# Performance work log

Hardware: AMD Instinct MI355X
Metric: run time of the kernel (lower is better)

## Reference

```python
import jax, jax.numpy as jnp
import numpy as np

B, N, D, H = 4, 2048, 768, 12
HD = D // H  # head_dim = 64


def setup_inputs() -> dict:
    key = jax.random.key(0)
    k1, k2, k3 = jax.random.split(key, 3)
    z = jax.random.normal(k1, (B, N, D), dtype=jnp.float32)
    # per-head qkv Linear weights, torch Linear convention: y = x @ W.T + b
    Wqkv = jax.random.normal(k2, (H, 3 * HD, D), dtype=jnp.float32) * 0.02
    bqkv = jnp.zeros((H, 3 * HD), dtype=jnp.float32)
    Wmsa = jax.random.normal(k3, (D, D), dtype=jnp.float32) * 0.02
    bmsa = jnp.zeros((D,), dtype=jnp.float32)
    return {"z": z, "Wqkv": Wqkv, "bqkv": bqkv, "Wmsa": Wmsa, "bmsa": bmsa}


def reference(z, Wqkv, bqkv, Wmsa, bmsa):
    # All heads' qkv projections in one einsum: [B,N,D] x [H,3hd,D] -> [B,H,N,3hd]
    qkv = jnp.einsum("bnd,hed->bhne", z, Wqkv) + bqkv[None, :, None, :]
    q, k, v = jnp.split(qkv, 3, axis=-1)  # each [B,H,N,hd]
    scale = 1.0 / jnp.sqrt(jnp.asarray(HD, dtype=z.dtype))
    scores = jnp.einsum("bhqd,bhkd->bhqk", q, k) * scale  # [B,H,N,N]
    attn = jax.nn.softmax(scores, axis=-1)
    out = jnp.einsum("bhqk,bhkd->bhqd", attn, v)  # [B,H,N,hd]
    # concat heads (head order matches the torch per-head cat)
    out = out.transpose(0, 2, 1, 3).reshape(B, N, H * HD)  # [B,N,D]
    return out @ Wmsa.T + bmsa
```

## Files before the change

kernel.cpp:

```cpp
#include <hip/hip_runtime.h>

typedef unsigned short u16;
typedef unsigned int u32;
typedef __attribute__((ext_vector_type(8))) short bf16x8;
typedef __attribute__((ext_vector_type(4))) float f32x4;

#define B_ 4
#define H_ 12
#define N_ 2048
#define D_ 768
#define HD_ 64
#define NTOK (B_ * N_)
#define NE   (H_ * 3 * HD_)

#define BM 128
#define BN 128
#define BK 64

#define QSCALE 0.18033688011112042f

__device__ __forceinline__ u16 f2bf(float f) {
    u32 u = __float_as_uint(f);
    u += 0x7fffu + ((u >> 16) & 1u);
    return (u16)(u >> 16);
}

__device__ __forceinline__ f32x4 mfma16(bf16x8 a, bf16x8 b, f32x4 c) {
    return __builtin_amdgcn_mfma_f32_16x16x32_bf16(a, b, c, 0, 0, 0);
}

__device__ __forceinline__ void g2l16(const u16* g, u16* l) {
    __builtin_amdgcn_global_load_lds(
        (const __attribute__((address_space(1))) void*)g,
        (__attribute__((address_space(3))) void*)l, 16, 0, 0);
}

__global__ __launch_bounds__(256) void cvt_bf16(const float* __restrict__ in,
                                                u16* __restrict__ out, int n4) {
    int i = blockIdx.x * blockDim.x + threadIdx.x;
    if (i < n4) {
        float4 v = ((const float4*)in)[i];
        u32 lo = (u32)f2bf(v.x) | ((u32)f2bf(v.y) << 16);
        u32 hi = (u32)f2bf(v.z) | ((u32)f2bf(v.w) << 16);
        ((uint2*)out)[i] = make_uint2(lo, hi);
    }
}

#define GEMM_CORE(Xp, Wp)                                                      \
    __shared__ u16 ldsA[BM * BK];                                              \
    __shared__ u16 ldsB[BN * BK];                                              \
    const int tid = threadIdx.x;                                               \
    const int wave = tid >> 6, lane = tid & 63;                                \
    const int lrow = lane & 15, quad = lane >> 4;                              \
    const int mbase = blockIdx.x * BM;                                         \
    const int nbase = blockIdx.y * BN;                                         \
    const int srow = tid >> 3;                                      \
    const int schunk = tid & 7;                                                \
    const int sk = (schunk ^ (srow & 7)) << 3;   \
    const int sdst = srow * BK + schunk * 8;     \
    const u16* gA = Xp + (size_t)(mbase + srow) * D_ + sk;                     \
    const u16* gB = Wp + (size_t)(nbase + srow) * D_ + sk;                     \
    const int m_ofs = (wave >> 1) * 64;                                        \
    const int n_ofs = (wave & 1) * 64;                                         \
    const int e_ = lrow & 7;                                                   \
    const int offA0 = (m_ofs + lrow) * BK + ((quad ^ e_) << 3);                \
    const int offB0 = (n_ofs + lrow) * BK + ((quad ^ e_) << 3);                \
    f32x4 acc[4][4] = {};                                                      \
    for (int kt = 0; kt < D_; kt += BK) {                                      \
        __syncthreads();                                                       \
        _Pragma("unroll") for (int i = 0; i < 4; i++) {                        \
            g2l16(gA + (size_t)(32 * i) * D_ + kt, ldsA + sdst + i * 32 * BK); \
            g2l16(gB + (size_t)(32 * i) * D_ + kt, ldsB + sdst + i * 32 * BK); \
        }                                                                      \
        __syncthreads();                                                       \
        _Pragma("unroll") for (int ks = 0; ks < 2; ks++) {                     \
            const int oa = offA0 ^ (ks << 5);                                  \
            const int ob = offB0 ^ (ks << 5);                                  \
            bf16x8 af[4], bfr[4];                                              \
            _Pragma("unroll") for (int c = 0; c < 4; c++)                      \
                af[c] = *(const bf16x8*)&ldsA[oa + c * 16 * BK];               \
            _Pragma("unroll") for (int c = 0; c < 4; c++)                      \
                bfr[c] = *(const bf16x8*)&ldsB[ob + c * 16 * BK];              \
            _Pragma("unroll") for (int i = 0; i < 4; i++)                      \
                _Pragma("unroll") for (int j = 0; j < 4; j++)                  \
                    acc[i][j] = mfma16(af[i], bfr[j], acc[i][j]);              \
        }                                                                      \
    }

__global__ __launch_bounds__(256) void gemm_qkv(const u16* __restrict__ X,
                                                const u16* __restrict__ W,
                                                const float* __restrict__ bqkv,
                                                u16* __restrict__ Qs,
                                                u16* __restrict__ Ks,
                                                u16* __restrict__ Vt) {
    GEMM_CORE(X, W)
#pragma unroll
    for (int cn = 0; cn < 4; cn++) {
        const int E = nbase + n_ofs + cn * 16;
        const int h = E / 192;
        const int rr = E - h * 192;
        const int kind = rr >> 6;
        const int d = (rr & 63) + lrow;
        const float bias = bqkv[E + lrow];
#pragma unroll
        for (int cm = 0; cm < 4; cm++) {
#pragma unroll
            for (int r = 0; r < 4; r++) {
                const int t = mbase + m_ofs + cm * 16 + quad * 4 + r;
                const int b_ = t >> 11, n = t & (N_ - 1);
                const size_t bh = (size_t)(b_ * H_ + h);
                const float val = acc[cm][cn][r] + bias;
                if (kind == 0) {
                    Qs[(bh * N_ + n) * HD_ + d] = f2bf(val * QSCALE);
                } else if (kind == 1) {
                    Ks[(bh * N_ + n) * HD_ + d] = f2bf(val);
                } else {
                    Vt[(bh * HD_ + d) * N_ + n] = f2bf(val);
                }
            }
        }
    }
}

__global__ __launch_bounds__(256) void gemm_out(const u16* __restrict__ X2,
                                                const u16* __restrict__ W,
                                                const float* __restrict__ bmsa,
                                                float* __restrict__ out) {
    GEMM_CORE(X2, W)
#pragma unroll
    for (int cn = 0; cn < 4; cn++) {
        const int col = nbase + n_ofs + cn * 16 + lrow;
        const float bias = bmsa[col];
#pragma unroll
        for (int cm = 0; cm < 4; cm++) {
#pragma unroll
            for (int r = 0; r < 4; r++) {
                const int t = mbase + m_ofs + cm * 16 + quad * 4 + r;
                out[(size_t)t * D_ + col] = acc[cm][cn][r] + bias;
            }
        }
    }
}

__global__ __launch_bounds__(256, 3) void flash_attn(const u16* __restrict__ Qs,
                                                     const u16* __restrict__ Ks,
                                                     const u16* __restrict__ Vt,
                                                     u16* __restrict__ X2) {
    __shared__ u16 ldsK[2][64 * HD_];
    __shared__ u16 ldsV[2][64 * HD_];
    __shared__ u16 ldsP[4][2][16][68];
    const int tid = threadIdx.x;
    const int wave = tid >> 6, lane = tid & 63;
    const int lrow = lane & 15, quad = lane >> 4;
    const int qbase = blockIdx.x * 128 + wave * 32;
    const int bh = blockIdx.y;
    const int b = bh / H_, h = bh - b * H_;

    const u16* Kb = Ks + (size_t)bh * N_ * HD_;
    const u16* Vb = Vt + (size_t)bh * HD_ * N_;

    const int srow = tid >> 3;
    const int schunk = tid & 7;
    const int skk = (schunk ^ (srow & 7)) << 3;
    const int sdst = srow * HD_ + schunk * 8;

    bf16x8 qa[2][2];
#pragma unroll
    for (int t = 0; t < 2; t++) {
        const u16* Qb = Qs + ((size_t)bh * N_ + qbase + t * 16 + lrow) * HD_ + quad * 8;
        qa[t][0] = *(const bf16x8*)(Qb);
        qa[t][1] = *(const bf16x8*)(Qb + 32);
    }

    const int fofs = (quad ^ (lrow & 7)) << 3;
    const short onebf = (short)0x3F80;
    const bf16x8 ones = {onebf, onebf, onebf, onebf, onebf, onebf, onebf, onebf};

    f32x4 Oacc[2][4] = {};
    f32x4 lacc[2] = {};

    {
        const u16* gK = Kb + (size_t)srow * HD_ + skk;
        g2l16(gK, &ldsK[0][sdst]);
        g2l16(gK + (size_t)32 * HD_, &ldsK[0][sdst + 32 * HD_]);
        const u16* gV = Vb + (size_t)srow * N_ + skk;
        g2l16(gV, &ldsV[0][sdst]);
        g2l16(gV + (size_t)32 * N_, &ldsV[0][sdst + 32 * HD_]);
    }

    for (int it = 0; it < N_ / 64; it++) {
        const int cur = it & 1;
        __syncthreads();
        if (it + 1 < N_ / 64) {
            const int kt2 = (it + 1) << 6;
            const u16* gK = Kb + (size_t)(kt2 + srow) * HD_ + skk;
            g2l16(gK, &ldsK[cur ^ 1][sdst]);
            g2l16(gK + (size_t)32 * HD_, &ldsK[cur ^ 1][sdst + 32 * HD_]);
            const u16* gV = Vb + (size_t)srow * N_ + kt2 + skk;
            g2l16(gV, &ldsV[cur ^ 1][sdst]);
            g2l16(gV + (size_t)32 * N_, &ldsV[cur ^ 1][sdst + 32 * HD_]);
        }
        bf16x8 kf[8];
#pragma unroll
        for (int c = 0; c < 4; c++) {
            const int o = (c * 16 + lrow) * HD_ + fofs;
            kf[2 * c]     = *(const bf16x8*)&ldsK[cur][o];
            kf[2 * c + 1] = *(const bf16x8*)&ldsK[cur][o ^ 32];
        }
        f32x4 s[2][4] = {};
#pragma unroll
        for (int t = 0; t < 2; t++)
#pragma unroll
            for (int c = 0; c < 4; c++) {
                s[t][c] = mfma16(kf[2 * c], qa[t][0], s[t][c]);
                s[t][c] = mfma16(kf[2 * c + 1], qa[t][1], s[t][c]);
            }
#pragma unroll
        for (int t = 0; t < 2; t++)
#pragma unroll
            for (int c = 0; c < 4; c++) {
                u32 a0 = __float_as_uint(__builtin_amdgcn_exp2f(s[t][c][0])) + 0x8000u;
                u32 a1 = __float_as_uint(__builtin_amdgcn_exp2f(s[t][c][1])) + 0x8000u;
                u32 a2 = __float_as_uint(__builtin_amdgcn_exp2f(s[t][c][2])) + 0x8000u;
                u32 a3 = __float_as_uint(__builtin_amdgcn_exp2f(s[t][c][3])) + 0x8000u;
                uint2 pk;
                pk.x = __builtin_amdgcn_perm(a1, a0, 0x07060302u);
                pk.y = __builtin_amdgcn_perm(a3, a2, 0x07060302u);
                *(uint2*)&ldsP[wave][t][lrow][c * 16 + quad * 4] = pk;
            }
        bf16x8 pa[2][2];
#pragma unroll
        for (int t = 0; t < 2; t++) {
            pa[t][0] = *(const bf16x8*)&ldsP[wave][t][lrow][quad * 8];
            pa[t][1] = *(const bf16x8*)&ldsP[wave][t][lrow][32 + quad * 8];
        }
#pragma unroll
        for (int t = 0; t < 2; t++) {
            lacc[t] = mfma16(pa[t][0], ones, lacc[t]);
            lacc[t] = mfma16(pa[t][1], ones, lacc[t]);
        }
#pragma unroll
        for (int c = 0; c < 4; c++) {
            const int o = (c * 16 + lrow) * HD_ + fofs;
            bf16x8 v0 = *(const bf16x8*)&ldsV[cur][o];
            bf16x8 v1 = *(const bf16x8*)&ldsV[cur][o ^ 32];
#pragma unroll
            for (int t = 0; t < 2; t++) {
                Oacc[t][c] = mfma16(pa[t][0], v0, Oacc[t][c]);
                Oacc[t][c] = mfma16(pa[t][1], v1, Oacc[t][c]);
            }
        }
    }
#pragma unroll
    for (int t = 0; t < 2; t++)
#pragma unroll
        for (int r = 0; r < 4; r++) {
            const float inv = 1.0f / lacc[t][r];
            const int qrow = qbase + t * 16 + quad * 4 + r;
#pragma unroll
            for (int c = 0; c < 4; c++) {
                X2[((size_t)b * N_ + qrow) * D_ + h * HD_ + c * 16 + lrow] =
                    f2bf(Oacc[t][c][r] * inv);
            }
        }
}

extern "C" void kernel_launch(void* const* d_in, const int* in_sizes, int n_in,
                              void* d_out, int out_size, void* d_ws, size_t ws_size,
                              hipStream_t stream) {
    const float* z    = (const float*)d_in[0];
    const float* Wqkv = (const float*)d_in[1];
    const float* bqkv = (const float*)d_in[2];
    const float* Wmsa = (const float*)d_in[3];
    const float* bmsa = (const float*)d_in[4];
    float* out = (float*)d_out;

    u16* Xbf = (u16*)d_ws;
    u16* Wqb = Xbf + (size_t)NTOK * D_;
    u16* Wmb = Wqb + (size_t)NE * D_;
    u16* Qs  = Wmb + (size_t)D_ * D_;
    u16* Ks  = Qs + (size_t)B_ * H_ * N_ * HD_;
    u16* Vt  = Ks + (size_t)B_ * H_ * N_ * HD_;
    u16* X2  = Vt + (size_t)B_ * H_ * N_ * HD_;

    const int nz = NTOK * D_ / 4;
    const int nwq = NE * D_ / 4;
    const int nwm = D_ * D_ / 4;
    cvt_bf16<<<(nz + 255) / 256, 256, 0, stream>>>(z, Xbf, nz);
    cvt_bf16<<<(nwq + 255) / 256, 256, 0, stream>>>(Wqkv, Wqb, nwq);
    cvt_bf16<<<(nwm + 255) / 256, 256, 0, stream>>>(Wmsa, Wmb, nwm);

    gemm_qkv<<<dim3(NTOK / BM, NE / BN), 256, 0, stream>>>(Xbf, Wqb, bqkv, Qs, Ks, Vt);
    flash_attn<<<dim3(N_ / 128, B_ * H_), 256, 0, stream>>>(Qs, Ks, Vt, X2);
    gemm_out<<<dim3(NTOK / BM, D_ / BN), 256, 0, stream>>>(X2, Wmb, bmsa, out);
}
```

Before: 228.9 us.

## Fuse bf16 conversions, stage QKV epilogue through LDS, shrink out-GEMM tile

The three fp32→bf16 conversion launches become one kernel that indexes across all three buffers. The QKV GEMM epilogue now stages the Q and K tiles in padded LDS and writes them as full 128-byte row vectors instead of scattered 2-byte stores. V^T is written as packed 8-byte chunks. The output GEMM uses 64-row tiles, doubling its block count for better occupancy across CUs at the cost of less reuse of the B operand.

Result: faster. 215.3 us (-6.0%).

```diff
diff --git a/kernel.cpp b/kernel.cpp
--- a/kernel.cpp
+++ b/kernel.cpp
@@ -13,9 +13,8 @@
 #define NTOK (B_ * N_)
 #define NE   (H_ * 3 * HD_)
 
-#define BM 128
-#define BN 128
 #define BK 64
+#define CPITCH 144
 
 #define QSCALE 0.18033688011112042f
 
@@ -35,53 +34,71 @@
         (__attribute__((address_space(3))) void*)l, 16, 0, 0);
 }
 
-__global__ __launch_bounds__(256) void cvt_bf16(const float* __restrict__ in,
-                                                u16* __restrict__ out, int n4) {
+#define NZ4  (NTOK * D_ / 4)
+#define NWQ4 (NE * D_ / 4)
+#define NWM4 (D_ * D_ / 4)
+__global__ __launch_bounds__(256) void cvt_all(const float* __restrict__ z,
+                                               const float* __restrict__ Wq,
+                                               const float* __restrict__ Wm,
+                                               u16* __restrict__ Xbf,
+                                               u16* __restrict__ Wqb,
+                                               u16* __restrict__ Wmb) {
     int i = blockIdx.x * blockDim.x + threadIdx.x;
-    if (i < n4) {
-        float4 v = ((const float4*)in)[i];
-        u32 lo = (u32)f2bf(v.x) | ((u32)f2bf(v.y) << 16);
-        u32 hi = (u32)f2bf(v.z) | ((u32)f2bf(v.w) << 16);
-        ((uint2*)out)[i] = make_uint2(lo, hi);
-    }
-}
-
-#define GEMM_CORE(Xp, Wp)                                                      \
-    __shared__ u16 ldsA[BM * BK];                                              \
-    __shared__ u16 ldsB[BN * BK];                                              \
+    const float* src;
+    u16* dst;
+    int j;
+    if (i < NZ4) {
+        src = z; dst = Xbf; j = i;
+    } else if (i < NZ4 + NWQ4) {
+        src = Wq; dst = Wqb; j = i - NZ4;
+    } else if (i < NZ4 + NWQ4 + NWM4) {
+        src = Wm; dst = Wmb; j = i - NZ4 - NWQ4;
+    } else {
+        return;
+    }
+    float4 v = ((const float4*)src)[j];
+    u32 lo = (u32)f2bf(v.x) | ((u32)f2bf(v.y) << 16);
+    u32 hi = (u32)f2bf(v.z) | ((u32)f2bf(v.w) << 16);
+    ((uint2*)dst)[j] = make_uint2(lo, hi);
+}
+
+#define GEMM_CORE(Xp, Wp, TM, SMELEMS)                                         \
+    __shared__ u16 smem[SMELEMS];                                              \
+    u16* ldsA = smem;                                                          \
+    u16* ldsB = smem + (TM) * BK;                                              \
     const int tid = threadIdx.x;                                               \
     const int wave = tid >> 6, lane = tid & 63;                                \
     const int lrow = lane & 15, quad = lane >> 4;                              \
-    const int mbase = blockIdx.x * BM;                                         \
-    const int nbase = blockIdx.y * BN;                                         \
+    const int mbase = blockIdx.x * (TM);                                       \
+    const int nbase = blockIdx.y * 128;                                        \
     const int srow = tid >> 3;                                      \
     const int schunk = tid & 7;                                                \
     const int sk = (schunk ^ (srow & 7)) << 3;   \
     const int sdst = srow * BK + schunk * 8;     \
     const u16* gA = Xp + (size_t)(mbase + srow) * D_ + sk;                     \
     const u16* gB = Wp + (size_t)(nbase + srow) * D_ + sk;                     \
-    const int m_ofs = (wave >> 1) * 64;                                        \
+    const int m_ofs = (wave >> 1) * ((TM) / 2);                                \
     const int n_ofs = (wave & 1) * 64;                                         \
     const int e_ = lrow & 7;                                                   \
     const int offA0 = (m_ofs + lrow) * BK + ((quad ^ e_) << 3);                \
     const int offB0 = (n_ofs + lrow) * BK + ((quad ^ e_) << 3);                \
-    f32x4 acc[4][4] = {};                                                      \
+    f32x4 acc[(TM) / 32][4] = {};                                              \
     for (int kt = 0; kt < D_; kt += BK) {                                      \
         __syncthreads();                                                       \
-        _Pragma("unroll") for (int i = 0; i < 4; i++) {                        \
+        _Pragma("unroll") for (int i = 0; i < (TM) / 32; i++)                  \
             g2l16(gA + (size_t)(32 * i) * D_ + kt, ldsA + sdst + i * 32 * BK); \
+        _Pragma("unroll") for (int i = 0; i < 4; i++)                          \
             g2l16(gB + (size_t)(32 * i) * D_ + kt, ldsB + sdst + i * 32 * BK); \
-        }                                                                      \
         __syncthreads();                                                       \
         _Pragma("unroll") for (int ks = 0; ks < 2; ks++) {                     \
             const int oa = offA0 ^ (ks << 5);                                  \
             const int ob = offB0 ^ (ks << 5);                                  \
-            bf16x8 af[4], bfr[4];                                              \
-            _Pragma("unroll") for (int c = 0; c < 4; c++)                      \
+            bf16x8 af[(TM) / 32], bfr[4];                                      \
+            _Pragma("unroll") for (int c = 0; c < (TM) / 32; c++)              \
                 af[c] = *(const bf16x8*)&ldsA[oa + c * 16 * BK];               \
             _Pragma("unroll") for (int c = 0; c < 4; c++)                      \
                 bfr[c] = *(const bf16x8*)&ldsB[ob + c * 16 * BK];              \
-            _Pragma("unroll") for (int i = 0; i < 4; i++)                      \
+            _Pragma("unroll") for (int i = 0; i < (TM) / 32; i++)              \
                 _Pragma("unroll") for (int j = 0; j < 4; j++)                  \
                     acc[i][j] = mfma16(af[i], bfr[j], acc[i][j]);              \
         }                                                                      \
@@ -93,31 +110,58 @@
                                                 u16* __restrict__ Qs,
                                                 u16* __restrict__ Ks,
                                                 u16* __restrict__ Vt) {
-    GEMM_CORE(X, W)
+    GEMM_CORE(X, W, 128, 128 * CPITCH)
+    __syncthreads();
+    u16* ldsC = smem;
 #pragma unroll
     for (int cn = 0; cn < 4; cn++) {
         const int E = nbase + n_ofs + cn * 16;
         const int h = E / 192;
         const int rr = E - h * 192;
         const int kind = rr >> 6;
-        const int d = (rr & 63) + lrow;
         const float bias = bqkv[E + lrow];
-#pragma unroll
-        for (int cm = 0; cm < 4; cm++) {
-#pragma unroll
-            for (int r = 0; r < 4; r++) {
-                const int t = mbase + m_ofs + cm * 16 + quad * 4 + r;
-                const int b_ = t >> 11, n = t & (N_ - 1);
+        if (kind == 2) {
+            const int d = (rr & 63) + lrow;
+#pragma unroll
+            for (int cm = 0; cm < 4; cm++) {
+                const int t0 = mbase + m_ofs + cm * 16 + quad * 4;
+                const int b_ = t0 >> 11, n0 = t0 & (N_ - 1);
                 const size_t bh = (size_t)(b_ * H_ + h);
-                const float val = acc[cm][cn][r] + bias;
-                if (kind == 0) {
-                    Qs[(bh * N_ + n) * HD_ + d] = f2bf(val * QSCALE);
-                } else if (kind == 1) {
-                    Ks[(bh * N_ + n) * HD_ + d] = f2bf(val);
-                } else {
-                    Vt[(bh * HD_ + d) * N_ + n] = f2bf(val);
+                uint2 pk;
+                pk.x = (u32)f2bf(acc[cm][cn][0] + bias) |
+                       ((u32)f2bf(acc[cm][cn][1] + bias) << 16);
+                pk.y = (u32)f2bf(acc[cm][cn][2] + bias) |
+                       ((u32)f2bf(acc[cm][cn][3] + bias) << 16);
+                *(uint2*)&Vt[(bh * HD_ + d) * N_ + n0] = pk;
+            }
+        } else {
+            const int fcol = n_ofs + cn * 16 + lrow;
+            const float scale = (kind == 0) ? QSCALE : 1.0f;
+#pragma unroll
+            for (int cm = 0; cm < 4; cm++)
+#pragma unroll
+                for (int r = 0; r < 4; r++) {
+                    const int tok = m_ofs + cm * 16 + quad * 4 + r;
+                    ldsC[tok * CPITCH + fcol] =
+                        f2bf((acc[cm][cn][r] + bias) * scale);
                 }
-            }
+        }
+    }
+    __syncthreads();
+    {
+        const int tok = tid >> 1, fh = tid & 1;
+        const int gf = nbase + fh * 64;
+        const int kind2 = (gf >> 6) % 3;
+        if (kind2 != 2) {
+            const int h2 = gf / 192;
+            const int t = mbase + tok;
+            const int b2 = t >> 11, n2 = t & (N_ - 1);
+            u16* dst = (kind2 == 0 ? Qs : Ks) +
+                       ((size_t)(b2 * H_ + h2) * N_ + n2) * HD_;
+            const u16* src = &ldsC[tok * CPITCH + fh * 64];
+#pragma unroll
+            for (int j = 0; j < 8; j++)
+                *(uint4*)&dst[j * 8] = *(const uint4*)&src[j * 8];
         }
     }
 }
@@ -126,13 +170,13 @@
                                                 const u16* __restrict__ W,
                                                 const float* __restrict__ bmsa,
                                                 float* __restrict__ out) {
-    GEMM_CORE(X2, W)
+    GEMM_CORE(X2, W, 64, (64 + 128) * BK)
 #pragma unroll
     for (int cn = 0; cn < 4; cn++) {
         const int col = nbase + n_ofs + cn * 16 + lrow;
         const float bias = bmsa[col];
 #pragma unroll
-        for (int cm = 0; cm < 4; cm++) {
+        for (int cm = 0; cm < 2; cm++) {
 #pragma unroll
             for (int r = 0; r < 4; r++) {
                 const int t = mbase + m_ofs + cm * 16 + quad * 4 + r;
@@ -283,14 +327,10 @@
     u16* Vt  = Ks + (size_t)B_ * H_ * N_ * HD_;
     u16* X2  = Vt + (size_t)B_ * H_ * N_ * HD_;
 
-    const int nz = NTOK * D_ / 4;
-    const int nwq = NE * D_ / 4;
-    const int nwm = D_ * D_ / 4;
-    cvt_bf16<<<(nz + 255) / 256, 256, 0, stream>>>(z, Xbf, nz);
-    cvt_bf16<<<(nwq + 255) / 256, 256, 0, stream>>>(Wqkv, Wqb, nwq);
-    cvt_bf16<<<(nwm + 255) / 256, 256, 0, stream>>>(Wmsa, Wmb, nwm);
-
-    gemm_qkv<<<dim3(NTOK / BM, NE / BN), 256, 0, stream>>>(Xbf, Wqb, bqkv, Qs, Ks, Vt);
+    const int ntot = NZ4 + NWQ4 + NWM4;
+    cvt_all<<<(ntot + 255) / 256, 256, 0, stream>>>(z, Wqkv, Wmsa, Xbf, Wqb, Wmb);
+
+    gemm_qkv<<<dim3(NTOK / 128, NE / 128), 256, 0, stream>>>(Xbf, Wqb, bqkv, Qs, Ks, Vt);
     flash_attn<<<dim3(N_ / 128, B_ * H_), 256, 0, stream>>>(Qs, Ks, Vt, X2);
-    gemm_out<<<dim3(NTOK / BM, D_ / BN), 256, 0, stream>>>(X2, Wmb, bmsa, out);
-}
+    gemm_out<<<dim3(NTOK / 64, D_ / 128), 256, 0, stream>>>(X2, Wmb, bmsa, out);
+}
```
